# Optimization experiments

Measured on AMD Instinct MI355X. Metric: run time of the kernel, lower is better.

Reference implementation:

```python
import jax, jax.numpy as jnp
import numpy as np

# 4D conv over (L, P, W, H) decomposed as k shifted 3D convs over (P, W, H),
# with the L spatial dim folded into the batch. Faithful to convNd(num_dims=4),
# stride 1, 'same' padding (padding = (k-1)//2), no bias.

def conv4d(x, w):
    # x: [B, C, L, P, W, H]; w: [O, I, k, k, k, k]
    k = w.shape[2]
    p = (k - 1) // 2
    B, C, L, P, Wd, Hd = x.shape
    O = w.shape[0]
    xp = jnp.pad(x, ((0, 0), (0, 0), (p, p), (0, 0), (0, 0), (0, 0)))
    dn = ('NCDHW', 'OIDHW', 'NCDHW')
    out = jnp.zeros((B, O, L, P, Wd, Hd), x.dtype)
    for dl in range(k):  # k <= 3, static loop over kernel taps along L
        xs = xp[:, :, dl:dl + L]                                  # [B,C,L,P,W,H]
        xs = xs.transpose(0, 2, 1, 3, 4, 5).reshape(B * L, C, P, Wd, Hd)
        y = jax.lax.conv_general_dilated(xs, w[:, :, dl], (1, 1, 1),
                                         [(p, p)] * 3, dimension_numbers=dn)
        out = out + y.reshape(B, L, O, P, Wd, Hd).transpose(0, 2, 1, 3, 4, 5)
    return out


def inception4d(x, weights):
    # mean over parallel 4D convs with kernel sizes 1, 3, ... (2i+1)
    acc = conv4d(x, weights[0])
    for w in weights[1:]:
        acc = acc + conv4d(x, w)
    return acc / len(weights)


def setup_inputs() -> dict:
    key = jax.random.key(0)
    ks = jax.random.split(key, 5)
    B, T, W, H, C = 4, 48, 8, 8, 32
    d_model, d_ff = 32, 64
    x = jax.random.normal(ks[0], (B, T, W, H, C), dtype=jnp.float32)
    # Inception_Block4D weights: kernel sizes 1 and 3 (num_kernels=2), no bias
    w1_0 = jax.random.normal(ks[1], (d_ff, d_model, 1, 1, 1, 1), dtype=jnp.float32) * 0.1
    w1_1 = jax.random.normal(ks[2], (d_ff, d_model, 3, 3, 3, 3), dtype=jnp.float32) * 0.02
    w2_0 = jax.random.normal(ks[3], (d_model, d_ff, 1, 1, 1, 1), dtype=jnp.float32) * 0.1
    w2_1 = jax.random.normal(ks[4], (d_model, d_ff, 3, 3, 3, 3), dtype=jnp.float32) * 0.02
    return {"x": x, "w1_0": w1_0, "w1_1": w1_1, "w2_0": w2_0, "w2_1": w2_1}


def reference(x, w1_0, w1_1, w2_0, w2_1):
    B, T, W, H, C = x.shape
    periods = (2, 3, 4)                       # FFT_for_Period hardcoded output
    xf = jnp.ones((B, len(periods)), x.dtype) # hardcoded uniform weights
    real_len = T                              # seq_len + pred_len
    res = []
    for period in periods:
        if real_len % period != 0:
            length = (real_len // period + 1) * period
            out = jnp.concatenate([x, x[:, -(length - real_len):]], axis=1)
        else:
            length = real_len
            out = x
        # [B, L, P, W, H, C] -> [B, C, L, P, W, H]
        out = out.reshape(B, length // period, period, W, H, C).transpose(0, 5, 1, 2, 3, 4)
        h = inception4d(out, [w1_0, w1_1])
        h = jax.nn.gelu(h, approximate=False)  # torch nn.GELU default (exact)
        h = inception4d(h, [w2_0, w2_1])
        # [B, C, L, P, W, H] -> [B, (L P), W, H, C]
        h = h.transpose(0, 2, 3, 4, 5, 1).reshape(B, length, W, H, C)
        res.append(h[:, :real_len])
    res = jnp.stack(res, axis=1)              # [B, k, T, W, H, C]
    pw = jax.nn.softmax(xf, axis=1).reshape(B, len(periods), 1, 1, 1, 1)
    return jnp.sum(res * pw, axis=1) + x
```

## Files before the change

kernel.cpp:

```cpp
#include <hip/hip_runtime.h>
#include <math.h>


typedef __attribute__((ext_vector_type(8))) short bf16x8;
typedef __attribute__((ext_vector_type(4))) float f32x4;
typedef unsigned short u16;

#define XC 3200
#define HC2 7168
#define XSEG 617600
#define ZSEG_END 639104
#define W1OFF 639104
#define W2OFF 804992
#define H1OFF 970880
#define H1P 1383424
#define PREP_N 970880
#define OUT_Q 98304
#define PREP_TOT (PREP_N + OUT_Q)

#define WAITVM(N) asm volatile("s_waitcnt vmcnt(" #N ")" ::: "memory")
#define SBAR()    asm volatile("s_barrier" ::: "memory")

__device__ __forceinline__ u16 f2bf(float f) {
    unsigned u = __float_as_uint(f);
    unsigned r = u + 0x7fffu + ((u >> 16) & 1u);
    return (u16)(r >> 16);
}
__device__ __forceinline__ float gelu_exact(float v) {
    return 0.5f * v * (1.0f + erff(v * 0.7071067811865476f));
}

__device__ __forceinline__ void cp1k(const u16* g, u16* l, int lane) {
    __builtin_amdgcn_global_load_lds(
        (const __attribute__((address_space(1))) unsigned int*)(g + lane * 8),
        (__attribute__((address_space(3))) unsigned int*)(l + lane * 8),
        16, 0, 0);
}

__global__ __launch_bounds__(256) void prep(
    const float* __restrict__ x,
    const float* __restrict__ w1_0, const float* __restrict__ w1_1,
    const float* __restrict__ w2_0, const float* __restrict__ w2_1,
    u16* __restrict__ ws, float* __restrict__ out) {
    int i = blockIdx.x * 256 + threadIdx.x;
    if (i < XSEG) {
        int cellidx = i / XC; int inner = i - cellidx * XC;
        int cellpos = inner >> 5; int low = inner & 31;
        int sc = low >> 3, jj = low & 7;
        int c = ((sc ^ (cellpos & 3)) << 3) + jj;
        int wp = cellpos / 10, hp = cellpos - (cellpos / 10) * 10;
        float v = 0.f;
        if (cellidx < 192 && wp >= 1 && wp <= 8 && hp >= 1 && hp <= 8)
            v = x[(cellidx * 64 + (wp - 1) * 8 + (hp - 1)) * 32 + c];
        ws[i] = f2bf(v);
    } else if (i < ZSEG_END) {
        int j = i - XSEG;
        int per = j / 7168; int off = j - per * 7168;
        ws[H1OFF + per * H1P + 192 * 7168 + off] = 0;
    } else if (i < W2OFF) {
        int j = i - W1OFF;
        int tap = j >> 11; int r = j & 2047;
        int nh = r >> 10; int rr = r & 1023;
        int chunkh = rr >> 3, jj = rr & 7;
        int m = chunkh & 15, nq = (chunkh >> 4) & 1, quad = chunkh >> 5;
        int o = nh * 32 + nq * 16 + m, c = quad * 8 + jj;
        float v = 0.5f * w1_1[(o * 32 + c) * 81 + tap];
        if (tap == 40) v += 0.5f * w1_0[o * 32 + c];
        ws[i] = f2bf(v);
    } else if (i < PREP_N) {
        int j = i - W2OFF;
        int tap = j >> 11; int r = j & 2047;
        int kh = r >> 10; int rr = r & 1023;
        int chunkh = rr >> 3, jj = rr & 7;
        int m = chunkh & 15, nt = (chunkh >> 4) & 1, quad = chunkh >> 5;
        int o = nt * 16 + m, c = kh * 32 + quad * 8 + jj;
        float v = 0.5f * w2_1[(o * 64 + c) * 81 + tap];
        if (tap == 40) v += 0.5f * w2_0[o * 64 + c];
        ws[i] = f2bf(v);
    } else if (i < PREP_TOT) {
        int j = i - PREP_N;
        ((float4*)out)[j] = ((const float4*)x)[j];
    }
}

__device__ __forceinline__ void decode240(int jid, int& per, int& bb,
                                          int& half, int& t0, int& sites) {
    int group = jid / 10, b = jid - group * 10;
    per = group >> 3; int rem = group & 7;
    bb = rem >> 1; half = rem & 1;
    if (b < 8) { t0 = 5 * b;            sites = 5; }
    else       { t0 = 40 + 4 * (b - 8); sites = 4; }
}

template<int P>
__device__ __forceinline__ void conv1_body(
    const u16* __restrict__ xs, const u16* __restrict__ w1b,
    u16* __restrict__ h1, int t0, int sites, int bb, int nh,
    u16* __restrict__ s_a, u16* __restrict__ s_w) {
    constexpr int HB = (P == 2) ? 0 : (P == 3) ? H1P : 2 * H1P;
    constexpr int L = 48 / P;
    constexpr int EXT = P + 1;
    const int NW = sites + 2 * EXT;
    const int NP = NW * 7;

    int tid = threadIdx.x;
    int lane = tid & 63, wv = tid >> 6;
    int m = lane & 15, quad = lane >> 4;
    int ts = wv >> 1, mh = wv & 1;
    int t = t0 + ts;
    int l = t / P, q = t - l * P;
    bool active = ts < sites;

    int sp[2];
#pragma unroll
    for (int mtl = 0; mtl < 2; ++mtl) {
        int pos = (mh * 2 + mtl) * 16 + m;
        sp[mtl] = (pos >> 3) * 10 + (pos & 7);
    }

    f32x4 acc[2][2];
#pragma unroll
    for (int mtl = 0; mtl < 2; ++mtl)
#pragma unroll
        for (int nq = 0; nq < 2; ++nq) acc[mtl][nq] = f32x4{0.f, 0.f, 0.f, 0.f};

    auto stageS = [&](int sg) {
        const u16* src = w1b + nh * 1024;
        u16* dst = s_w + (sg & 1) * 9216;
#pragma unroll
        for (int i = 0; i < 2; ++i) {
            int k = wv * 2 + i; if (k >= 18) k = 17;
            cp1k(src + (sg * 9 + (k >> 1)) * 2048 + (k & 1) * 512,
                 dst + k * 512, lane);
        }
    };

    for (int p = wv; p < NP; p += 12) {
        int si = p / 7, pc = p - si * 7;
        int tt = t0 - EXT + si;
        if ((unsigned)tt < 48u)
            cp1k(xs + (bb * 48 + tt) * XC + pc * 512,
                 s_a + si * 3584 + pc * 512, lane);
    }
    stageS(0);
    WAITVM(0); SBAR();

#pragma unroll 1
    for (int g = 0; g < 9; ++g) {
        if (g < 8) stageS(g + 1);

        int dl = g / 3, dq = g - dl * 3;
        int lq = l + dl - 1, qq = q + dq - 1;
        bool valid = active && ((unsigned)lq < (unsigned)L) &&
                     ((unsigned)qq < (unsigned)P);
        if (valid) {
            int si = ts + dl * P + dq;
            const u16* ba = s_a + si * 3584;
            const u16* bw = s_w + (g & 1) * 9216;
#pragma unroll
            for (int dw = 0; dw < 3; ++dw)
#pragma unroll
                for (int j = 0; j < 3; ++j) {
                    const u16* tw = bw + (dw * 3 + j) * 1024;
                    bf16x8 wf0 = *(const bf16x8*)(tw +
                        (((quad * 2 + 0) * 16 + m) << 3));
                    bf16x8 wf1 = *(const bf16x8*)(tw +
                        (((quad * 2 + 1) * 16 + m) << 3));
#pragma unroll
                    for (int mtl = 0; mtl < 2; ++mtl) {
                        int cellpos = sp[mtl] + dw * 10 + j;
                        bf16x8 af = *(const bf16x8*)(ba + cellpos * 32 +
                            ((quad ^ (cellpos & 3)) << 3));
                        acc[mtl][0] = __builtin_amdgcn_mfma_f32_16x16x32_bf16(
                            af, wf0, acc[mtl][0], 0, 0, 0);
                        acc[mtl][1] = __builtin_amdgcn_mfma_f32_16x16x32_bf16(
                            af, wf1, acc[mtl][1], 0, 0, 0);
                    }
                }
        }
        if (g < 8) { WAITVM(0); SBAR(); }
    }

    if (active) {
        u16* hh = h1 + HB + (bb * 48 + t) * HC2 + nh * 3584;
#pragma unroll
        for (int mtl = 0; mtl < 2; ++mtl)
#pragma unroll
            for (int r = 0; r < 4; ++r) {
                int pos = (mh * 2 + mtl) * 16 + quad * 4 + r;
                int cellpos = ((pos >> 3) + 1) * 10 + (pos & 7) + 1;
#pragma unroll
                for (int nq = 0; nq < 2; ++nq) {
                    int ol = nq * 16 + m;
                    hh[cellpos * 32 + (((ol >> 3) ^ (cellpos & 3)) << 3) +
                       (ol & 7)] = f2bf(gelu_exact(acc[mtl][nq][r]));
                }
            }
    }
#pragma unroll
    for (int it = 0; it < 5; ++it) {
        int k = it * 768 + tid;
        if (k < sites * 576) {
            int tc = k / 576; int rr = k - tc * 576;
            int bp = rr >> 4, u = rr & 15;
            int cp;
            if (bp < 10) cp = bp;
            else if (bp < 20) cp = 90 + (bp - 10);
            else if (bp < 28) cp = (bp - 19) * 10;
            else cp = (bp - 27) * 10 + 9;
            unsigned int* h32 = (unsigned int*)(h1 + HB +
                (bb * 48 + t0 + tc) * HC2 + nh * 3584);
            h32[cp * 16 + u] = 0;
        }
    }
}

__global__ __launch_bounds__(768) void conv1_k(
    const u16* __restrict__ ws_x, const u16* __restrict__ ws_w1,
    u16* __restrict__ ws_h1) {
    __shared__ __align__(16) u16 s_a[15 * 3584];
    __shared__ __align__(16) u16 s_w[2 * 9216];
    int g = blockIdx.x;
    int jid = (g & 7) * 30 + (g >> 3);
    int per, bb, nh, t0, sites;
    decode240(jid, per, bb, nh, t0, sites);
    if (per == 0)
        conv1_body<2>(ws_x, ws_w1, ws_h1, t0, sites, bb, nh, s_a, s_w);
    else if (per == 1)
        conv1_body<3>(ws_x, ws_w1, ws_h1, t0, sites, bb, nh, s_a, s_w);
    else
        conv1_body<4>(ws_x, ws_w1, ws_h1, t0, sites, bb, nh, s_a, s_w);
}

template<int P>
__device__ __forceinline__ void conv2_body(
    const u16* __restrict__ h1, const u16* __restrict__ w2b,
    float* __restrict__ out, int t0, int sites, int bb, int kh,
    u16* __restrict__ s_a, u16* __restrict__ s_w) {
    constexpr int HB = (P == 2) ? 0 : (P == 3) ? H1P : 2 * H1P;
    constexpr int L = 48 / P;
    constexpr int EXT = P + 1;
    const int NW = sites + 2 * EXT;
    const int NP = NW * 7;

    int tid = threadIdx.x;
    int lane = tid & 63, wv = tid >> 6;
    int m = lane & 15, quad = lane >> 4;
    int ts = wv >> 1, mh = wv & 1;
    int t = t0 + ts;
    int l = t / P, q = t - l * P;
    const u16* hb = h1 + HB;
    bool active = ts < sites;

    int sp[2];
#pragma unroll
    for (int mtl = 0; mtl < 2; ++mtl) {
        int pos = (mh * 2 + mtl) * 16 + m;
        sp[mtl] = (pos >> 3) * 10 + (pos & 7);
    }

    f32x4 acc[2][2];
#pragma unroll
    for (int mtl = 0; mtl < 2; ++mtl)
#pragma unroll
        for (int nt = 0; nt < 2; ++nt) acc[mtl][nt] = f32x4{0.f, 0.f, 0.f, 0.f};

    auto stageS = [&](int sg) {
        const u16* src = w2b + kh * 1024;
        u16* dst = s_w + (sg & 1) * 9216;
#pragma unroll
        for (int i = 0; i < 2; ++i) {
            int k = wv * 2 + i; if (k >= 18) k = 17;
            cp1k(src + (sg * 9 + (k >> 1)) * 2048 + (k & 1) * 512,
                 dst + k * 512, lane);
        }
    };

    for (int p = wv; p < NP; p += 12) {
        int si = p / 7, pc = p - si * 7;
        int tt = t0 - EXT + si;
        if ((unsigned)tt < 48u)
            cp1k(hb + (bb * 48 + tt) * HC2 + kh * 3584 + pc * 512,
                 s_a + si * 3584 + pc * 512, lane);
    }
    stageS(0);
    WAITVM(0); SBAR();

#pragma unroll 1
    for (int g = 0; g < 9; ++g) {
        if (g < 8) stageS(g + 1);

        int dl = g / 3, dq = g - dl * 3;
        int lq = l + dl - 1, qq = q + dq - 1;
        bool valid = active && ((unsigned)lq < (unsigned)L) &&
                     ((unsigned)qq < (unsigned)P);
        if (valid) {
            int si = ts + dl * P + dq;
            const u16* ba = s_a + si * 3584;
            const u16* bw = s_w + (g & 1) * 9216;
#pragma unroll
            for (int dw = 0; dw < 3; ++dw)
#pragma unroll
                for (int j = 0; j < 3; ++j) {
                    const u16* tw = bw + (dw * 3 + j) * 1024;
                    bf16x8 wf0 = *(const bf16x8*)(tw +
                        (((quad * 2 + 0) * 16 + m) << 3));
                    bf16x8 wf1 = *(const bf16x8*)(tw +
                        (((quad * 2 + 1) * 16 + m) << 3));
#pragma unroll
                    for (int mtl = 0; mtl < 2; ++mtl) {
                        int cellpos = sp[mtl] + dw * 10 + j;
                        bf16x8 af = *(const bf16x8*)(ba + cellpos * 32 +
                            ((quad ^ (cellpos & 3)) << 3));
                        acc[mtl][0] = __builtin_amdgcn_mfma_f32_16x16x32_bf16(
                            af, wf0, acc[mtl][0], 0, 0, 0);
                        acc[mtl][1] = __builtin_amdgcn_mfma_f32_16x16x32_bf16(
                            af, wf1, acc[mtl][1], 0, 0, 0);
                    }
                }
        }
        if (g < 8) { WAITVM(0); SBAR(); }
    }

    if (active) {
        float* orow = out + (bb * 48 + t) * 2048;
        const float s = 1.0f / 3.0f;
#pragma unroll
        for (int mtl = 0; mtl < 2; ++mtl)
#pragma unroll
            for (int nt = 0; nt < 2; ++nt)
#pragma unroll
                for (int r = 0; r < 4; ++r) {
                    int pos = (mh * 2 + mtl) * 16 + quad * 4 + r;
                    atomicAdd(&orow[pos * 32 + nt * 16 + m],
                              acc[mtl][nt][r] * s);
                }
    }
}

__global__ __launch_bounds__(768) void conv2_k(
    const u16* __restrict__ ws_h1, const u16* __restrict__ ws_w2,
    float* __restrict__ out) {
    __shared__ __align__(16) u16 s_a[15 * 3584];
    __shared__ __align__(16) u16 s_w[2 * 9216];
    int g = blockIdx.x;
    int jid = (g & 7) * 30 + (g >> 3);
    int per, bb, kh, t0, sites;
    decode240(jid, per, bb, kh, t0, sites);
    if (per == 0)
        conv2_body<2>(ws_h1, ws_w2, out, t0, sites, bb, kh, s_a, s_w);
    else if (per == 1)
        conv2_body<3>(ws_h1, ws_w2, out, t0, sites, bb, kh, s_a, s_w);
    else
        conv2_body<4>(ws_h1, ws_w2, out, t0, sites, bb, kh, s_a, s_w);
}

extern "C" void kernel_launch(void* const* d_in, const int* in_sizes, int n_in,
                              void* d_out, int out_size, void* d_ws, size_t ws_size,
                              hipStream_t stream) {
    const float* x    = (const float*)d_in[0];
    const float* w1_0 = (const float*)d_in[1];
    const float* w1_1 = (const float*)d_in[2];
    const float* w2_0 = (const float*)d_in[3];
    const float* w2_1 = (const float*)d_in[4];
    float* out = (float*)d_out;

    u16* ws = (u16*)d_ws;
    u16* ws_x  = ws;
    u16* ws_w1 = ws + W1OFF;
    u16* ws_w2 = ws + W2OFF;
    u16* ws_h1 = ws + H1OFF;

    prep<<<(PREP_TOT + 255) / 256, 256, 0, stream>>>(
        x, w1_0, w1_1, w2_0, w2_1, ws, out);
    conv1_k<<<240, 768, 0, stream>>>(ws_x, ws_w1, ws_h1);
    conv2_k<<<240, 768, 0, stream>>>(ws_h1, ws_w2, out);
}
```

Baseline: 106.2 us.

## Load conv weights directly into registers with double-buffered prefetch, dropping LDS staging

```diff
diff --git a/kernel.cpp b/kernel.cpp
--- a/kernel.cpp
+++ b/kernel.cpp
@@ -96,7 +96,7 @@
 __device__ __forceinline__ void conv1_body(
     const u16* __restrict__ xs, const u16* __restrict__ w1b,
     u16* __restrict__ h1, int t0, int sites, int bb, int nh,
-    u16* __restrict__ s_a, u16* __restrict__ s_w) {
+    u16* __restrict__ s_a) {
     constexpr int HB = (P == 2) ? 0 : (P == 3) ? H1P : 2 * H1P;
     constexpr int L = 48 / P;
     constexpr int EXT = P + 1;
@@ -124,17 +124,6 @@
 #pragma unroll
         for (int nq = 0; nq < 2; ++nq) acc[mtl][nq] = f32x4{0.f, 0.f, 0.f, 0.f};
 
-    auto stageS = [&](int sg) {
-        const u16* src = w1b + nh * 1024;
-        u16* dst = s_w + (sg & 1) * 9216;
-#pragma unroll
-        for (int i = 0; i < 2; ++i) {
-            int k = wv * 2 + i; if (k >= 18) k = 17;
-            cp1k(src + (sg * 9 + (k >> 1)) * 2048 + (k & 1) * 512,
-                 dst + k * 512, lane);
-        }
-    };
-
     for (int p = wv; p < NP; p += 12) {
         int si = p / 7, pc = p - si * 7;
         int tt = t0 - EXT + si;
@@ -142,46 +131,55 @@
             cp1k(xs + (bb * 48 + tt) * XC + pc * 512,
                  s_a + si * 3584 + pc * 512, lane);
     }
-    stageS(0);
     WAITVM(0); SBAR();
 
-#pragma unroll 1
-    for (int g = 0; g < 9; ++g) {
-        if (g < 8) stageS(g + 1);
-
-        int dl = g / 3, dq = g - dl * 3;
-        int lq = l + dl - 1, qq = q + dq - 1;
-        bool valid = active && ((unsigned)lq < (unsigned)L) &&
-                     ((unsigned)qq < (unsigned)P);
-        if (valid) {
+    if (active) {
+        const u16* wlane = w1b + nh * 1024 + ((quad * 32 + m) << 3);
+
+        bf16x8 wA[3][2], wB[3][2];
+        auto loadsub = [&](int s, bf16x8 (&w)[3][2]) {
+            const u16* tw = wlane + s * 3 * 2048;
+#pragma unroll
+            for (int j = 0; j < 3; ++j) {
+                w[j][0] = *(const bf16x8*)(tw + j * 2048);
+                w[j][1] = *(const bf16x8*)(tw + j * 2048 + 128);
+            }
+        };
+        auto csub = [&](int s, bf16x8 (&w)[3][2]) {
+            int g = s / 3, dw = s - g * 3;
+            int dl = g / 3, dq = g - dl * 3;
+            int lq = l + dl - 1, qq = q + dq - 1;
+            bool valid = ((unsigned)lq < (unsigned)L) &&
+                         ((unsigned)qq < (unsigned)P);
+            if (!valid) return;
             int si = ts + dl * P + dq;
             const u16* ba = s_a + si * 3584;
-            const u16* bw = s_w + (g & 1) * 9216;
-#pragma unroll
-            for (int dw = 0; dw < 3; ++dw)
-#pragma unroll
-                for (int j = 0; j < 3; ++j) {
-                    const u16* tw = bw + (dw * 3 + j) * 1024;
-                    bf16x8 wf0 = *(const bf16x8*)(tw +
-                        (((quad * 2 + 0) * 16 + m) << 3));
-                    bf16x8 wf1 = *(const bf16x8*)(tw +
-                        (((quad * 2 + 1) * 16 + m) << 3));
-#pragma unroll
-                    for (int mtl = 0; mtl < 2; ++mtl) {
-                        int cellpos = sp[mtl] + dw * 10 + j;
-                        bf16x8 af = *(const bf16x8*)(ba + cellpos * 32 +
-                            ((quad ^ (cellpos & 3)) << 3));
-                        acc[mtl][0] = __builtin_amdgcn_mfma_f32_16x16x32_bf16(
-                            af, wf0, acc[mtl][0], 0, 0, 0);
-                        acc[mtl][1] = __builtin_amdgcn_mfma_f32_16x16x32_bf16(
-                            af, wf1, acc[mtl][1], 0, 0, 0);
-                    }
+#pragma unroll
+            for (int j = 0; j < 3; ++j) {
+#pragma unroll
+                for (int mtl = 0; mtl < 2; ++mtl) {
+                    int cellpos = sp[mtl] + dw * 10 + j;
+                    bf16x8 af = *(const bf16x8*)(ba + cellpos * 32 +
+                                                 ((quad ^ (cellpos & 3)) << 3));
+                    acc[mtl][0] = __builtin_amdgcn_mfma_f32_16x16x32_bf16(
+                        af, w[j][0], acc[mtl][0], 0, 0, 0);
+                    acc[mtl][1] = __builtin_amdgcn_mfma_f32_16x16x32_bf16(
+                        af, w[j][1], acc[mtl][1], 0, 0, 0);
                 }
+            }
+        };
+
+        loadsub(0, wA); loadsub(1, wB);
+#pragma unroll 1
+        for (int su = 0; su < 27; su += 2) {
+            csub(su, wA);
+            if (su + 2 < 27) loadsub(su + 2, wA);
+            if (su + 1 < 27) {
+                csub(su + 1, wB);
+                if (su + 3 < 27) loadsub(su + 3, wB);
+            }
         }
-        if (g < 8) { WAITVM(0); SBAR(); }
-    }
-
-    if (active) {
+
         u16* hh = h1 + HB + (bb * 48 + t) * HC2 + nh * 3584;
 #pragma unroll
         for (int mtl = 0; mtl < 2; ++mtl)
@@ -219,24 +217,23 @@
     const u16* __restrict__ ws_x, const u16* __restrict__ ws_w1,
     u16* __restrict__ ws_h1) {
     __shared__ __align__(16) u16 s_a[15 * 3584];
-    __shared__ __align__(16) u16 s_w[2 * 9216];
     int g = blockIdx.x;
     int jid = (g & 7) * 30 + (g >> 3);
     int per, bb, nh, t0, sites;
     decode240(jid, per, bb, nh, t0, sites);
     if (per == 0)
-        conv1_body<2>(ws_x, ws_w1, ws_h1, t0, sites, bb, nh, s_a, s_w);
+        conv1_body<2>(ws_x, ws_w1, ws_h1, t0, sites, bb, nh, s_a);
     else if (per == 1)
-        conv1_body<3>(ws_x, ws_w1, ws_h1, t0, sites, bb, nh, s_a, s_w);
+        conv1_body<3>(ws_x, ws_w1, ws_h1, t0, sites, bb, nh, s_a);
     else
-        conv1_body<4>(ws_x, ws_w1, ws_h1, t0, sites, bb, nh, s_a, s_w);
+        conv1_body<4>(ws_x, ws_w1, ws_h1, t0, sites, bb, nh, s_a);
 }
 
 template<int P>
 __device__ __forceinline__ void conv2_body(
     const u16* __restrict__ h1, const u16* __restrict__ w2b,
     float* __restrict__ out, int t0, int sites, int bb, int kh,
-    u16* __restrict__ s_a, u16* __restrict__ s_w) {
+    u16* __restrict__ s_a) {
     constexpr int HB = (P == 2) ? 0 : (P == 3) ? H1P : 2 * H1P;
     constexpr int L = 48 / P;
     constexpr int EXT = P + 1;
@@ -265,17 +262,6 @@
 #pragma unroll
         for (int nt = 0; nt < 2; ++nt) acc[mtl][nt] = f32x4{0.f, 0.f, 0.f, 0.f};
 
-    auto stageS = [&](int sg) {
-        const u16* src = w2b + kh * 1024;
-        u16* dst = s_w + (sg & 1) * 9216;
-#pragma unroll
-        for (int i = 0; i < 2; ++i) {
-            int k = wv * 2 + i; if (k >= 18) k = 17;
-            cp1k(src + (sg * 9 + (k >> 1)) * 2048 + (k & 1) * 512,
-                 dst + k * 512, lane);
-        }
-    };
-
     for (int p = wv; p < NP; p += 12) {
         int si = p / 7, pc = p - si * 7;
         int tt = t0 - EXT + si;
@@ -283,46 +269,55 @@
             cp1k(hb + (bb * 48 + tt) * HC2 + kh * 3584 + pc * 512,
                  s_a + si * 3584 + pc * 512, lane);
     }
-    stageS(0);
     WAITVM(0); SBAR();
 
-#pragma unroll 1
-    for (int g = 0; g < 9; ++g) {
-        if (g < 8) stageS(g + 1);
-
-        int dl = g / 3, dq = g - dl * 3;
-        int lq = l + dl - 1, qq = q + dq - 1;
-        bool valid = active && ((unsigned)lq < (unsigned)L) &&
-                     ((unsigned)qq < (unsigned)P);
-        if (valid) {
+    if (active) {
+        const u16* wlane = w2b + kh * 1024 + ((quad * 32 + m) << 3);
+
+        bf16x8 wA[3][2], wB[3][2];
+        auto loadsub = [&](int s, bf16x8 (&w)[3][2]) {
+            const u16* tw = wlane + s * 3 * 2048;
+#pragma unroll
+            for (int j = 0; j < 3; ++j) {
+                w[j][0] = *(const bf16x8*)(tw + j * 2048);
+                w[j][1] = *(const bf16x8*)(tw + j * 2048 + 128);
+            }
+        };
+        auto csub = [&](int s, bf16x8 (&w)[3][2]) {
+            int g = s / 3, dw = s - g * 3;
+            int dl = g / 3, dq = g - dl * 3;
+            int lq = l + dl - 1, qq = q + dq - 1;
+            bool valid = ((unsigned)lq < (unsigned)L) &&
+                         ((unsigned)qq < (unsigned)P);
+            if (!valid) return;
             int si = ts + dl * P + dq;
             const u16* ba = s_a + si * 3584;
-            const u16* bw = s_w + (g & 1) * 9216;
-#pragma unroll
-            for (int dw = 0; dw < 3; ++dw)
-#pragma unroll
-                for (int j = 0; j < 3; ++j) {
-                    const u16* tw = bw + (dw * 3 + j) * 1024;
-                    bf16x8 wf0 = *(const bf16x8*)(tw +
-                        (((quad * 2 + 0) * 16 + m) << 3));
-                    bf16x8 wf1 = *(const bf16x8*)(tw +
-                        (((quad * 2 + 1) * 16 + m) << 3));
-#pragma unroll
-                    for (int mtl = 0; mtl < 2; ++mtl) {
-                        int cellpos = sp[mtl] + dw * 10 + j;
-                        bf16x8 af = *(const bf16x8*)(ba + cellpos * 32 +
-                            ((quad ^ (cellpos & 3)) << 3));
-                        acc[mtl][0] = __builtin_amdgcn_mfma_f32_16x16x32_bf16(
-                            af, wf0, acc[mtl][0], 0, 0, 0);
-                        acc[mtl][1] = __builtin_amdgcn_mfma_f32_16x16x32_bf16(
-                            af, wf1, acc[mtl][1], 0, 0, 0);
-                    }
+#pragma unroll
+            for (int j = 0; j < 3; ++j) {
+#pragma unroll
+                for (int mtl = 0; mtl < 2; ++mtl) {
+                    int cellpos = sp[mtl] + dw * 10 + j;
+                    bf16x8 af = *(const bf16x8*)(ba + cellpos * 32 +
+                                                 ((quad ^ (cellpos & 3)) << 3));
+                    acc[mtl][0] = __builtin_amdgcn_mfma_f32_16x16x32_bf16(
+                        af, w[j][0], acc[mtl][0], 0, 0, 0);
+                    acc[mtl][1] = __builtin_amdgcn_mfma_f32_16x16x32_bf16(
+                        af, w[j][1], acc[mtl][1], 0, 0, 0);
                 }
+            }
+        };
+
+        loadsub(0, wA); loadsub(1, wB);
+#pragma unroll 1
+        for (int su = 0; su < 27; su += 2) {
+            csub(su, wA);
+            if (su + 2 < 27) loadsub(su + 2, wA);
+            if (su + 1 < 27) {
+                csub(su + 1, wB);
+                if (su + 3 < 27) loadsub(su + 3, wB);
+            }
         }
-        if (g < 8) { WAITVM(0); SBAR(); }
-    }
-
-    if (active) {
+
         float* orow = out + (bb * 48 + t) * 2048;
         const float s = 1.0f / 3.0f;
 #pragma unroll
@@ -342,17 +337,16 @@
     const u16* __restrict__ ws_h1, const u16* __restrict__ ws_w2,
     float* __restrict__ out) {
     __shared__ __align__(16) u16 s_a[15 * 3584];
-    __shared__ __align__(16) u16 s_w[2 * 9216];
     int g = blockIdx.x;
     int jid = (g & 7) * 30 + (g >> 3);
     int per, bb, kh, t0, sites;
     decode240(jid, per, bb, kh, t0, sites);
     if (per == 0)
-        conv2_body<2>(ws_h1, ws_w2, out, t0, sites, bb, kh, s_a, s_w);
+        conv2_body<2>(ws_h1, ws_w2, out, t0, sites, bb, kh, s_a);
     else if (per == 1)
-        conv2_body<3>(ws_h1, ws_w2, out, t0, sites, bb, kh, s_a, s_w);
+        conv2_body<3>(ws_h1, ws_w2, out, t0, sites, bb, kh, s_a);
     else
-        conv2_body<4>(ws_h1, ws_w2, out, t0, sites, bb, kh, s_a, s_w);
+        conv2_body<4>(ws_h1, ws_w2, out, t0, sites, bb, kh, s_a);
 }
 
 extern "C" void kernel_launch(void* const* d_in, const int* in_sizes, int n_in,
```

Result: slower. 115.3 us (+8.5%).
